# Kernel tuning notes

Hardware: AMD Instinct MI355X
Metric: run time of the kernel (lower is better)

## Reference

```python
import jax, jax.numpy as jnp
import numpy as np

HIDDEN_DIM = 400
STACK_DEPTH = 32
BATCH = 1
SEQ_LEN = 8192


def setup_inputs() -> dict:
    key = jax.random.key(0)
    k1, k2, k3 = jax.random.split(key, 3)
    hidden_state = jax.random.normal(k1, (BATCH, SEQ_LEN, HIDDEN_DIM), dtype=jnp.float32)
    # action_predictor: nn.Linear(hidden_dim, 3)
    W_ap = jax.random.normal(k2, (3, HIDDEN_DIM), dtype=jnp.float32) * 0.05
    b_ap = jnp.zeros((3,), dtype=jnp.float32)
    # D: nn.Parameter(torch.randn(1, hidden_dim))
    D = jax.random.normal(k3, (1, HIDDEN_DIM), dtype=jnp.float32)
    return {"hidden_state": hidden_state, "W_ap": W_ap, "b_ap": b_ap, "D": D}


def reference(hidden_state, W_ap, b_ap, D):
    # hidden_state: [B, T, H]
    B, T, H = hidden_state.shape
    # Per-step action probabilities (computed for all t at once): [B, T, 3]
    probs = jax.nn.softmax(jnp.einsum('bth,ah->bta', hidden_state, W_ap) + b_ap, axis=-1)
    # push value: sigmoid(D . h_t), scalar per (b, t) (well-defined at B=1)
    pv = jax.nn.sigmoid(jnp.einsum('bth,h->bt', hidden_state, D[0]))  # [B, T]
    push = jnp.transpose(probs[..., 0])   # [T, B]
    pop_ = jnp.transpose(probs[..., 1])   # [T, B]
    noop = jnp.transpose(probs[..., 2])   # [T, B]
    pv_t = jnp.transpose(pv)              # [T, B]

    stack0 = jnp.zeros((B, STACK_DEPTH, H), dtype=hidden_state.dtype)

    # Net effect of the two aliased in-place shifts (snapshot semantics):
    #   s2[0] = s[1]; s2[i] = s[i] for i >= 1
    # then stack[0] = push*push_val + pop*s2[1] + noop*s2[0]
    #               = push*push_val + (pop+noop)*s[1]
    def step(stack, xs):
        pu, po, no, v = xs  # each [B]
        s1 = stack[:, 1, :]  # [B, H]
        new_top = (pu * v)[:, None] + (po + no)[:, None] * s1  # [B, H]
        new_stack = stack.at[:, 0, :].set(new_top)
        return new_stack, new_stack

    _, stacks = jax.lax.scan(step, stack0, (push, pop_, noop, pv_t))  # [T, B, D, H]
    return jnp.transpose(stacks, (1, 0, 2, 3))  # [B, T, D, H]
```

## Files before the change

### kernel.cpp

```cpp
#include <hip/hip_runtime.h>

#define HDIM  400
#define TLEN  8192
#define DEPTH 32
#define SLICE  (DEPTH * HDIM)
#define SLICE4 (SLICE / 4)
#define ROW4   (HDIM / 4)
#define VBLOCK 256
#define FBLOCK 320

__global__ __launch_bounds__(VBLOCK) void val_kernel(
    const float* __restrict__ hs,
    const float* __restrict__ W,
    const float* __restrict__ b,
    const float* __restrict__ D,
    float* __restrict__ val)
{
    const int wave = threadIdx.x >> 6;
    const int lane = threadIdx.x & 63;
    const int t = blockIdx.x * (VBLOCK / 64) + wave;

    const float* __restrict__ x = hs + (size_t)t * HDIM;

    float a0 = 0.f, a1 = 0.f, a2 = 0.f, ad = 0.f;
    for (int i = lane; i < HDIM; i += 64) {
        float h = x[i];
        a0 += h * W[i];
        a1 += h * W[HDIM + i];
        a2 += h * W[2 * HDIM + i];
        ad += h * D[i];
    }

    #pragma unroll
    for (int off = 32; off > 0; off >>= 1) {
        a0 += __shfl_xor(a0, off);
        a1 += __shfl_xor(a1, off);
        a2 += __shfl_xor(a2, off);
        ad += __shfl_xor(ad, off);
    }

    float l0 = a0 + b[0];
    float l1 = a1 + b[1];
    float l2 = a2 + b[2];
    float m  = fmaxf(l0, fmaxf(l1, l2));
    float e0 = __expf(l0 - m);
    float e1 = __expf(l1 - m);
    float e2 = __expf(l2 - m);
    float p0 = e0 / (e0 + e1 + e2);
    float pv = 1.0f / (1.0f + __expf(-ad));
    float v  = p0 * pv;

    if (lane == 0) val[t] = v;
}

__global__ __launch_bounds__(FBLOCK) void fill_kernel(
    const float* __restrict__ val,
    float4* __restrict__ out)
{
    const int t = blockIdx.x;
    const float vt = val[t];
    float4* __restrict__ o = out + (size_t)t * SLICE4 + threadIdx.x;

    const float v0 = (threadIdx.x < ROW4) ? vt : 0.f;
    o[0] = make_float4(v0, v0, v0, v0);
    const float4 z = make_float4(0.f, 0.f, 0.f, 0.f);
    #pragma unroll
    for (int k = 1; k < SLICE4 / FBLOCK; ++k) {
        o[(size_t)k * FBLOCK] = z;
    }
}

extern "C" void kernel_launch(void* const* d_in, const int* in_sizes, int n_in,
                              void* d_out, int out_size, void* d_ws, size_t ws_size,
                              hipStream_t stream) {
    const float* hs = (const float*)d_in[0];
    const float* W  = (const float*)d_in[1];
    const float* b  = (const float*)d_in[2];
    const float* D  = (const float*)d_in[3];
    float* out = (float*)d_out;
    float* val = (float*)d_ws;

    val_kernel<<<TLEN / (VBLOCK / 64), VBLOCK, 0, stream>>>(hs, W, b, D, val);
    fill_kernel<<<TLEN, FBLOCK, 0, stream>>>(val, (float4*)out);
}
```

Before: 429.0 us.

## Fuse value computation into fill kernel and use nontemporal stores

Merges the per-timestep value kernel into the output fill kernel. The first two waves of each block compute the dot products and softmax/sigmoid redundantly per block, which removes one launch and the workspace round trip. The zero-heavy output writes also switch to nontemporal stores to reduce cache pollution on the large output. In exchange, the first 100 threads must finish the reduction before writing their slice, which could delay those stores.

```diff
diff --git a/kernel.cpp b/kernel.cpp
--- a/kernel.cpp
+++ b/kernel.cpp
@@ -6,67 +6,63 @@
 #define SLICE  (DEPTH * HDIM)
 #define SLICE4 (SLICE / 4)
 #define ROW4   (HDIM / 4)
-#define VBLOCK 256
 #define FBLOCK 320
 
-__global__ __launch_bounds__(VBLOCK) void val_kernel(
+typedef float float4x __attribute__((ext_vector_type(4)));
+
+__device__ __forceinline__ void nt_store(float4x* p, float4x v) {
+    __builtin_nontemporal_store(v, p);
+}
+
+__global__ __launch_bounds__(FBLOCK) void stack_fused_kernel(
     const float* __restrict__ hs,
     const float* __restrict__ W,
     const float* __restrict__ b,
     const float* __restrict__ D,
-    float* __restrict__ val)
+    float4x* __restrict__ out)
 {
+    const int t    = blockIdx.x;
     const int wave = threadIdx.x >> 6;
     const int lane = threadIdx.x & 63;
-    const int t = blockIdx.x * (VBLOCK / 64) + wave;
 
-    const float* __restrict__ x = hs + (size_t)t * HDIM;
-
-    float a0 = 0.f, a1 = 0.f, a2 = 0.f, ad = 0.f;
-    for (int i = lane; i < HDIM; i += 64) {
-        float h = x[i];
-        a0 += h * W[i];
-        a1 += h * W[HDIM + i];
-        a2 += h * W[2 * HDIM + i];
-        ad += h * D[i];
+    float v0 = 0.f;
+    if (wave < 2) {
+        const float* __restrict__ x = hs + (size_t)t * HDIM;
+        float a0 = 0.f, a1 = 0.f, a2 = 0.f, ad = 0.f;
+        for (int i = lane; i < HDIM; i += 64) {
+            float h = x[i];
+            a0 += h * W[i];
+            a1 += h * W[HDIM + i];
+            a2 += h * W[2 * HDIM + i];
+            ad += h * D[i];
+        }
+        #pragma unroll
+        for (int off = 32; off > 0; off >>= 1) {
+            a0 += __shfl_xor(a0, off);
+            a1 += __shfl_xor(a1, off);
+            a2 += __shfl_xor(a2, off);
+            ad += __shfl_xor(ad, off);
+        }
+        float l0 = a0 + b[0];
+        float l1 = a1 + b[1];
+        float l2 = a2 + b[2];
+        float m  = fmaxf(l0, fmaxf(l1, l2));
+        float e0 = __expf(l0 - m);
+        float e1 = __expf(l1 - m);
+        float e2 = __expf(l2 - m);
+        float p0 = e0 / (e0 + e1 + e2);
+        float pv = 1.0f / (1.0f + __expf(-ad));
+        float v  = p0 * pv;
+        v0 = (threadIdx.x < ROW4) ? v : 0.f;
     }
 
-    #pragma unroll
-    for (int off = 32; off > 0; off >>= 1) {
-        a0 += __shfl_xor(a0, off);
-        a1 += __shfl_xor(a1, off);
-        a2 += __shfl_xor(a2, off);
-        ad += __shfl_xor(ad, off);
-    }
-
-    float l0 = a0 + b[0];
-    float l1 = a1 + b[1];
-    float l2 = a2 + b[2];
-    float m  = fmaxf(l0, fmaxf(l1, l2));
-    float e0 = __expf(l0 - m);
-    float e1 = __expf(l1 - m);
-    float e2 = __expf(l2 - m);
-    float p0 = e0 / (e0 + e1 + e2);
-    float pv = 1.0f / (1.0f + __expf(-ad));
-    float v  = p0 * pv;
-
-    if (lane == 0) val[t] = v;
-}
-
-__global__ __launch_bounds__(FBLOCK) void fill_kernel(
-    const float* __restrict__ val,
-    float4* __restrict__ out)
-{
-    const int t = blockIdx.x;
-    const float vt = val[t];
-    float4* __restrict__ o = out + (size_t)t * SLICE4 + threadIdx.x;
-
-    const float v0 = (threadIdx.x < ROW4) ? vt : 0.f;
-    o[0] = make_float4(v0, v0, v0, v0);
-    const float4 z = make_float4(0.f, 0.f, 0.f, 0.f);
+    float4x* __restrict__ o = out + (size_t)t * SLICE4 + threadIdx.x;
+    float4x vv = { v0, v0, v0, v0 };
+    nt_store(&o[0], vv);
+    float4x z = { 0.f, 0.f, 0.f, 0.f };
     #pragma unroll
     for (int k = 1; k < SLICE4 / FBLOCK; ++k) {
-        o[(size_t)k * FBLOCK] = z;
+        nt_store(&o[(size_t)k * FBLOCK], z);
     }
 }
 
@@ -77,9 +73,7 @@
     const float* W  = (const float*)d_in[1];
     const float* b  = (const float*)d_in[2];
     const float* D  = (const float*)d_in[3];
-    float* out = (float*)d_out;
-    float* val = (float*)d_ws;
+    float4x* out = (float4x*)d_out;
 
-    val_kernel<<<TLEN / (VBLOCK / 64), VBLOCK, 0, stream>>>(hs, W, b, D, val);
-    fill_kernel<<<TLEN, FBLOCK, 0, stream>>>(val, (float4*)out);
+    stack_fused_kernel<<<TLEN, FBLOCK, 0, stream>>>(hs, W, b, D, out);
 }
```

Result: no change. 430.5 us (+0.3%).
